# Performance work log

Measured on AMD Instinct MI355X. Metric: run time of the kernel, lower is better.

The kernel has to match this reference:

```python
import jax, jax.numpy as jnp
import numpy as np

N = 100000
E = 1600000
IN_C = 32
HID = 64
OUT_C = 32


def setup_inputs() -> dict:
    key = jax.random.key(0)
    k1, k2, k3, k4, k5, k6 = jax.random.split(key, 6)
    x = jax.random.normal(k1, (N, IN_C), dtype=jnp.float32)
    edge_index = jax.random.randint(k2, (2, E), 0, N, dtype=jnp.int64)
    # MLP params: Linear(2*in, 64) -> ReLU -> Linear(64, out)
    s1 = 1.0 / np.sqrt(2 * IN_C)
    s2 = 1.0 / np.sqrt(HID)
    W1 = jax.random.uniform(k3, (2 * IN_C, HID), jnp.float32, -s1, s1)
    b1 = jax.random.uniform(k4, (HID,), jnp.float32, -s1, s1)
    W2 = jax.random.uniform(k5, (HID, OUT_C), jnp.float32, -s2, s2)
    b2 = jax.random.uniform(k6, (OUT_C,), jnp.float32, -s2, s2)
    return {"x": x, "edge_index": edge_index, "W1": W1, "b1": b1, "W2": W2, "b2": b2}


def reference(x, edge_index, W1, b1, W2, b2):
    # PyG EdgeConv: message = nn(cat([x_i, x_j - x_i])), aggr = max over incoming edges
    src = edge_index[0]  # j (neighbor)
    dst = edge_index[1]  # i (center / target node)
    x_i = x[dst]                      # [E, C]
    x_j = x[src]                      # [E, C]
    m = jnp.concatenate([x_i, x_j - x_i], axis=-1)       # [E, 2C]
    h = jnp.maximum(m @ W1 + b1, 0.0) @ W2 + b2          # [E, OUT_C]
    out = jax.ops.segment_max(h, dst, num_segments=x.shape[0])  # [N, OUT_C]
    # nodes with no incoming edges: segment_max yields -inf; PyG fills 0
    out = jnp.where(jnp.isfinite(out), out, 0.0)
    return out
```

## Files before the change

kernel.cpp:

```cpp
#include <hip/hip_runtime.h>

typedef unsigned int u32;
typedef __attribute__((ext_vector_type(8))) _Float16 half8v;
typedef __attribute__((ext_vector_type(4))) u32 u32x4;
typedef __attribute__((ext_vector_type(4))) float f32x4;

#define NPB1 128
#define SH1  7
#define NPB2 32
#define SH2  5
#define CHP  4096

__device__ __forceinline__ u32 enc_f32(float f) {
    u32 b = __float_as_uint(f);
    return (b & 0x80000000u) ? ~b : (b | 0x80000000u);
}
__device__ __forceinline__ float dec_f32(u32 u) {
    u32 b = (u & 0x80000000u) ? (u & 0x7FFFFFFFu) : ~u;
    return __uint_as_float(b);
}
__device__ __forceinline__ u32 pk_addrelu(u32 a, u32 b) {
    u32 r;
    asm("v_pk_add_f16 %0, %1, %2\n\tv_pk_max_f16 %0, %0, 0"
        : "=v"(r) : "v"(a), "v"(b));
    return r;
}
__device__ __forceinline__ u32 pkrtz(float lo, float hi) {
    auto h = __builtin_amdgcn_cvt_pkrtz(lo, hi);
    return __builtin_bit_cast(u32, h);
}

__global__ __launch_bounds__(256) void k_pq_hist(
    const float* __restrict__ x, const float* __restrict__ W1, const float* __restrict__ b1,
    const int* __restrict__ ei,
    u32* __restrict__ Pb, u32* __restrict__ Qb, u32* __restrict__ g1,
    int N, int E, int NSB1, int npc)
{
    __shared__ u32 smem[4224];
    int tid = threadIdx.x;
    int bid = (int)blockIdx.x;

    if (bid < npc) {
        u32* cnt = smem;
        for (int s = tid; s < NSB1; s += 256) cnt[s] = 0;
        __syncthreads();
        int s0 = bid * CHP, end = min(E, s0 + CHP);
        int nq = (end - s0) >> 2;
        const int4* d4p = (const int4*)(ei + (size_t)E + s0);
        for (int qi = tid; qi < nq; qi += 256) {
            int4 d4 = d4p[qi];
            atomicAdd(&cnt[d4.x >> SH1], 1u);
            atomicAdd(&cnt[d4.y >> SH1], 1u);
            atomicAdd(&cnt[d4.z >> SH1], 1u);
            atomicAdd(&cnt[d4.w >> SH1], 1u);
        }
        __syncthreads();
        for (int s = tid; s < NSB1; s += 256) g1[(size_t)s * npc + bid] = cnt[s];
        return;
    }

    float* sWTa = (float*)smem;
    float* sWTb = (float*)smem + 2048;
    for (int idx = tid; idx < 2048; idx += 256) {
        int j = idx >> 5, k = idx & 31;
        float a = W1[k * 64 + j];
        float b = W1[(k + 32) * 64 + j];
        sWTa[j * 32 + k] = a - b;
        sWTb[j * 32 + k] = b;
    }
    __syncthreads();

    int blk = bid - npc;
    int n = blk * 256 + tid;

    u32 pw[32], qw[32];
    if (n < N) {
        float xr[32];
        const float4* x4 = reinterpret_cast<const float4*>(x + (size_t)n * 32);
#pragma unroll
        for (int q = 0; q < 8; ++q) {
            float4 v = x4[q];
            xr[4 * q] = v.x; xr[4 * q + 1] = v.y; xr[4 * q + 2] = v.z; xr[4 * q + 3] = v.w;
        }
        for (int j0 = 0; j0 < 64; j0 += 2) {
            float pv[2], qv[2];
#pragma unroll
            for (int m = 0; m < 2; ++m) {
                int j = j0 + m;
                float a = b1[j], q = 0.f;
                const f32x4* wa4 = (const f32x4*)(sWTa + j * 32);
                const f32x4* wb4 = (const f32x4*)(sWTb + j * 32);
#pragma unroll
                for (int k4 = 0; k4 < 8; ++k4) {
                    f32x4 wa = wa4[k4];
                    f32x4 wb = wb4[k4];
#pragma unroll
                    for (int e = 0; e < 4; ++e) {
                        a = fmaf(xr[4 * k4 + e], wa[e], a);
                        q = fmaf(xr[4 * k4 + e], wb[e], q);
                    }
                }
                pv[m] = a; qv[m] = q;
            }
            pw[j0 >> 1] = pkrtz(pv[0], pv[1]);
            qw[j0 >> 1] = pkrtz(qv[0], qv[1]);
        }
    }
    __syncthreads();

    u32* sP = smem;
    u32* sQ = smem + 2112;
    for (int r = 0; r < 4; ++r) {
        if ((tid >> 6) == r && n < N) {
            int row = tid & 63;
#pragma unroll
            for (int i = 0; i < 32; ++i) {
                sP[row * 33 + i] = pw[i];
                sQ[row * 33 + i] = qw[i];
            }
        }
        __syncthreads();
        int nodebase = blk * 256 + r * 64;
        size_t wbase = (size_t)nodebase * 32;
        for (int w = tid; w < 2048; w += 256) {
            int node = nodebase + (w >> 5);
            if (node < N) {
                u32 v = sP[(w >> 5) * 33 + (w & 31)];
                u32 u = sQ[(w >> 5) * 33 + (w & 31)];
                Pb[wbase + w] = v;
                Qb[wbase + w] = u;
            }
        }
        __syncthreads();
    }
}

__global__ __launch_bounds__(256) void k_scan1(const u32* __restrict__ deg, u32* __restrict__ cursor,
                                               u32* __restrict__ bsum, int M) {
    __shared__ u32 sh[256];
    int t = threadIdx.x;
    int base = blockIdx.x * 2048 + t * 8;
    u32 v[8];
    if (base + 7 < M) {
        uint4 a = *reinterpret_cast<const uint4*>(deg + base);
        uint4 b = *reinterpret_cast<const uint4*>(deg + base + 4);
        v[0] = a.x; v[1] = a.y; v[2] = a.z; v[3] = a.w;
        v[4] = b.x; v[5] = b.y; v[6] = b.z; v[7] = b.w;
    } else {
#pragma unroll
        for (int i = 0; i < 8; ++i) v[i] = (base + i < M) ? deg[base + i] : 0;
    }
    u32 s = 0;
#pragma unroll
    for (int i = 0; i < 8; ++i) s += v[i];
    sh[t] = s; __syncthreads();
    u32 acc = s;
    for (int off = 1; off < 256; off <<= 1) {
        u32 add = (t >= off) ? sh[t - off] : 0;
        __syncthreads();
        acc += add; sh[t] = acc;
        __syncthreads();
    }
    u32 run = acc - s;
#pragma unroll
    for (int i = 0; i < 8; ++i) {
        if (base + i < M) cursor[base + i] = run;
        run += v[i];
    }
    if (t == 255) bsum[blockIdx.x] = acc;
}

__global__ __launch_bounds__(256) void k_scan2(const u32* __restrict__ bsum, u32* __restrict__ bsumX, int nb) {
    __shared__ u32 sh[256];
    int t = threadIdx.x;
    u32 v = (t < nb) ? bsum[t] : 0;
    sh[t] = v; __syncthreads();
    u32 acc = v;
    for (int off = 1; off < 256; off <<= 1) {
        u32 add = (t >= off) ? sh[t - off] : 0;
        __syncthreads();
        acc += add; sh[t] = acc;
        __syncthreads();
    }
    if (t < nb) bsumX[t] = acc - v;
}

__global__ __launch_bounds__(1024) void k_sp1(const int* __restrict__ ei,
                                              const u32* __restrict__ g1cur, const u32* __restrict__ bsumX1,
                                              u32* __restrict__ sorted, int E, int NSB1, int npc) {
    __shared__ u32 sb[1024], cnt[1024];
    int tid = threadIdx.x;
    int c = (int)blockIdx.x;
    for (int s = tid; s < NSB1; s += 1024) {
        size_t idx = (size_t)s * npc + c;
        sb[s] = g1cur[idx] + bsumX1[idx >> 11];
        cnt[s] = 0;
    }
    __syncthreads();
    int s0 = c * CHP, end = min(E, s0 + CHP);
    int nq = (end - s0) >> 2;
    const int4* d4p = (const int4*)(ei + (size_t)E + s0);
    const int4* s4p = (const int4*)(ei + s0);
    for (int qi = tid; qi < nq; qi += 1024) {
        int4 d4 = d4p[qi];
        int4 s4 = s4p[qi];
        int dd[4] = {d4.x, d4.y, d4.z, d4.w};
        int ss[4] = {s4.x, s4.y, s4.z, s4.w};
#pragma unroll
        for (int u = 0; u < 4; ++u) {
            int s = dd[u] >> SH1;
            u32 r = atomicAdd(&cnt[s], 1u);
            sorted[sb[s] + r] = (u32)ss[u] | ((u32)(dd[u] & (NPB1 - 1)) << 17);
        }
    }
}

__global__ __launch_bounds__(256) void k_sp2(const u32* __restrict__ sorted,
                                             const u32* __restrict__ g1cur, const u32* __restrict__ bsumX1,
                                             u32* __restrict__ sorted2, u32* __restrict__ base32,
                                             int E, int NSB1, int npc) {
    __shared__ u32 sb[4];
    __shared__ u32 cnt[4];
    int b = (int)blockIdx.x;
    int tid = threadIdx.x;

    size_t i0 = (size_t)b * npc;
    u32 start = g1cur[i0] + bsumX1[i0 >> 11];
    u32 bend;
    if (b + 1 < NSB1) {
        size_t i1 = (size_t)(b + 1) * npc;
        bend = g1cur[i1] + bsumX1[i1 >> 11];
    } else {
        bend = (u32)E;
    }

    if (tid < 4) cnt[tid] = 0;
    __syncthreads();

    for (u32 i = start + tid; i < bend; i += 256) {
        u32 rec = sorted[i];
        atomicAdd(&cnt[(rec >> 22) & 3u], 1u);
    }
    __syncthreads();

    if (tid == 0) {
        u32 run = start;
#pragma unroll
        for (int q = 0; q < 4; ++q) {
            sb[q] = run;
            base32[b * 4 + q] = run;
            run += cnt[q];
            cnt[q] = 0;
        }
    }
    __syncthreads();

    for (u32 i0b = start; i0b < bend; i0b += 256) {
        u32 i = i0b + tid;
        bool vld = i < bend;
        u32 rec = vld ? sorted[i] : 0u;
        int q = vld ? (int)((rec >> 22) & 3u) : -1;
#pragma unroll
        for (int qq = 0; qq < 4; ++qq) {
            unsigned long long m = __ballot(q == qq);
            if (m) {
                int prefix = __popcll(m & ((1ull << (tid & 63)) - 1ull));
                u32 wb;
                if ((tid & 63) == 0) wb = atomicAdd(&cnt[qq], (u32)__popcll(m));
                wb = __shfl(wb, 0, 64);
                if (q == qq) sorted2[sb[qq] + wb + prefix] = rec & 0x3FFFFFu;
            }
        }
    }
}

__global__ __launch_bounds__(512) void k_bucket(
    const u32* __restrict__ Pb, const u32* __restrict__ Qb,
    const u32* __restrict__ sorted2, const u32* __restrict__ base32,
    const float* __restrict__ W2, const float* __restrict__ b2,
    float* __restrict__ out, int E, int N, int NSB2)
{
    __shared__ u32 agg[NPB2 * 32];
    __shared__ u32 sPb[NPB2 * 32];
    int b = (int)blockIdx.x;
    int tid = threadIdx.x;
    int nodebase = b << SH2;

    for (int i = tid; i < NPB2 * 32; i += 512) agg[i] = 0u;
    for (int i = tid; i < NPB2 * 32; i += 512) {
        int loc = i >> 5, w = i & 31;
        int node = nodebase + loc;
        u32 v = (node < N) ? Pb[(size_t)node * 32 + w] : 0u;
        sPb[loc * 32 + ((((w >> 2) ^ (loc & 7)) << 2) | (w & 3))] = v;
    }

    int lane = tid & 63;
    int wid = tid >> 6;
    int n = lane & 15;
    int kc = lane >> 4;

    half8v b00, b01, b10, b11;
#pragma unroll
    for (int j = 0; j < 8; ++j) {
        int k = kc * 8 + j;
        b00[j] = (_Float16)W2[k * 32 + n];
        b01[j] = (_Float16)W2[(k + 32) * 32 + n];
        b10[j] = (_Float16)W2[k * 32 + n + 16];
        b11[j] = (_Float16)W2[(k + 32) * 32 + n + 16];
    }

    u32 start = base32[b];
    u32 bend  = (b + 1 < NSB2) ? base32[b + 1] : (u32)E;
    int ntiles = ((int)(bend - start) + 15) >> 4;

    __syncthreads();

    int t = wid;
    u32 slotA = start + (u32)t * 16u + (u32)n;
    u32 recA = 0;
    uint4 qA0, qA1;
    if (t < ntiles) {
        u32 sl = slotA < bend ? slotA : bend - 1;
        recA = sorted2[sl];
        int src = (int)(recA & 0x1FFFFu);
        const u32* qr = Qb + (size_t)src * 32;
        qA0 = *(const uint4*)(qr + kc * 4);
        qA1 = *(const uint4*)(qr + 16 + kc * 4);
    }

    for (; t < ntiles; t += 8) {
        u32 slotB = start + (u32)(t + 8) * 16u + (u32)n;
        u32 slB = slotB < bend ? slotB : bend - 1;
        u32 recB = sorted2[slB];
        int srcB = (int)(recB & 0x1FFFFu);
        const u32* qrB = Qb + (size_t)srcB * 32;
        uint4 qB0 = *(const uint4*)(qrB + kc * 4);
        uint4 qB1 = *(const uint4*)(qrB + 16 + kc * 4);

        bool valid = slotA < bend;
        int locA = (int)(recA >> 17);
        int local = valid ? locA : -1;

        const u32* pr = sPb + locA * 32;
        uint4 pA0 = *(const uint4*)(pr + ((kc ^ (locA & 7)) << 2));
        uint4 pA1 = *(const uint4*)(pr + (((4 + kc) ^ (locA & 7)) << 2));

        u32x4 aw0, aw1;
        aw0[0] = pk_addrelu(pA0.x, qA0.x);
        aw0[1] = pk_addrelu(pA0.y, qA0.y);
        aw0[2] = pk_addrelu(pA0.z, qA0.z);
        aw0[3] = pk_addrelu(pA0.w, qA0.w);
        aw1[0] = pk_addrelu(pA1.x, qA1.x);
        aw1[1] = pk_addrelu(pA1.y, qA1.y);
        aw1[2] = pk_addrelu(pA1.z, qA1.z);
        aw1[3] = pk_addrelu(pA1.w, qA1.w);
        half8v a0 = __builtin_bit_cast(half8v, aw0);
        half8v a1 = __builtin_bit_cast(half8v, aw1);

        f32x4 d0 = {0.f, 0.f, 0.f, 0.f};
        f32x4 d1 = {0.f, 0.f, 0.f, 0.f};
        d0 = __builtin_amdgcn_mfma_f32_16x16x32_f16(a0, b00, d0, 0, 0, 0);
        d0 = __builtin_amdgcn_mfma_f32_16x16x32_f16(a1, b01, d0, 0, 0, 0);
        d1 = __builtin_amdgcn_mfma_f32_16x16x32_f16(a0, b10, d1, 0, 0, 0);
        d1 = __builtin_amdgcn_mfma_f32_16x16x32_f16(a1, b11, d1, 0, 0, 0);

#pragma unroll
        for (int i = 0; i < 4; ++i) {
            int r = kc * 4 + i;
            int lr = __shfl(local, r, 64);
            if (lr >= 0) {
                int sw = (lr & 1) << 4;
                atomicMax(&agg[(lr << 5) + (n ^ sw)], enc_f32(d0[i]));
                atomicMax(&agg[(lr << 5) + ((n + 16) ^ sw)], enc_f32(d1[i]));
            }
        }

        slotA = slotB; recA = recB;
        qA0 = qB0; qA1 = qB1;
    }

    __syncthreads();
    for (int i = tid; i < NPB2 * 32; i += 512) {
        int local = i >> 5, c = i & 31;
        int node = nodebase + local;
        if (node < N) {
            u32 u = agg[(local << 5) + (c ^ ((local & 1) << 4))];
            out[(size_t)node * 32 + c] = u ? (dec_f32(u) + b2[c]) : 0.f;
        }
    }
}

__global__ __launch_bounds__(256) void fb_edge(const float* __restrict__ x, const int* __restrict__ ei,
                                               const float* __restrict__ W1, const float* __restrict__ b1,
                                               const float* __restrict__ W2, const float* __restrict__ b2,
                                               u32* __restrict__ out, int E) {
    int e = blockIdx.x * 256 + threadIdx.x;
    if (e >= E) return;
    int src = ei[e], dst = ei[E + e];
    float m[64];
    const float4* xi4 = reinterpret_cast<const float4*>(x + (size_t)dst * 32);
    const float4* xj4 = reinterpret_cast<const float4*>(x + (size_t)src * 32);
#pragma unroll
    for (int q = 0; q < 8; ++q) {
        float4 a = xi4[q], b = xj4[q];
        m[q * 4] = a.x; m[q * 4 + 1] = a.y; m[q * 4 + 2] = a.z; m[q * 4 + 3] = a.w;
        m[32 + q * 4] = b.x - a.x; m[32 + q * 4 + 1] = b.y - a.y;
        m[32 + q * 4 + 2] = b.z - a.z; m[32 + q * 4 + 3] = b.w - a.w;
    }
    float acc[32];
#pragma unroll
    for (int c = 0; c < 32; ++c) acc[c] = b2[c];
    for (int j = 0; j < 64; ++j) {
        float h = b1[j];
#pragma unroll
        for (int k = 0; k < 64; ++k) h = fmaf(m[k], W1[k * 64 + j], h);
        h = fmaxf(h, 0.0f);
#pragma unroll
        for (int c = 0; c < 32; ++c) acc[c] = fmaf(h, W2[j * 32 + c], acc[c]);
    }
    u32* o = out + (size_t)dst * 32;
#pragma unroll
    for (int c = 0; c < 32; ++c) atomicMax(o + c, enc_f32(acc[c]));
}
__global__ __launch_bounds__(256) void fb_decode(u32* __restrict__ buf, int n) {
    int i = blockIdx.x * 256 + threadIdx.x;
    if (i >= n) return;
    u32 u = buf[i];
    reinterpret_cast<float*>(buf)[i] = u ? dec_f32(u) : 0.f;
}

extern "C" void kernel_launch(void* const* d_in, const int* in_sizes, int n_in,
                              void* d_out, int out_size, void* d_ws, size_t ws_size,
                              hipStream_t stream) {
    const float* x  = (const float*)d_in[0];
    const int*   ei = (const int*)d_in[1];
    const float* W1 = (const float*)d_in[2];
    const float* b1 = (const float*)d_in[3];
    const float* W2 = (const float*)d_in[4];
    const float* b2 = (const float*)d_in[5];

    int N = in_sizes[0] / 32;
    int E = in_sizes[1] / 2;
    int NSB1 = (N + NPB1 - 1) >> SH1;
    int NSB2 = NSB1 * 4;
    int npc = (E + CHP - 1) / CHP;
    int M1  = NSB1 * npc;
    int nb1 = (M1 + 2047) / 2048;

    char* ws = (char*)d_ws;
    size_t off = 0;
    auto alloc = [&](size_t bytes) { char* p = ws + off; off += (bytes + 255) & ~(size_t)255; return p; };
    u32*   Pb      = (u32*)alloc((size_t)N * 32 * 4);
    u32*   Qb      = (u32*)alloc((size_t)N * 32 * 4);
    u32*   g1      = (u32*)alloc((size_t)M1 * 4);
    u32*   g1cur   = (u32*)alloc((size_t)M1 * 4);
    u32*   bsum1   = (u32*)alloc(256 * 4);
    u32*   bsumX1  = (u32*)alloc(256 * 4);
    u32*   base32  = (u32*)alloc((size_t)(NSB2 + 1) * 4);
    u32*   sorted  = (u32*)alloc((size_t)E * 4);
    u32*   sorted2 = (u32*)alloc((size_t)E * 4);
    bool fits = (off <= ws_size) && (NSB1 <= 1024) &&
                (N < (1 << 17)) && ((E & 3) == 0) && (nb1 <= 256);

    if (!fits) {
        hipMemsetAsync(d_out, 0, (size_t)out_size * 4, stream);
        int be = (E + 255) / 256;
        fb_edge<<<be, 256, 0, stream>>>(x, ei, W1, b1, W2, b2, (u32*)d_out, E);
        fb_decode<<<(out_size + 255) / 256, 256, 0, stream>>>((u32*)d_out, out_size);
        return;
    }

    int pq_blocks = (N + 255) / 256;
    k_pq_hist<<<npc + pq_blocks, 256, 0, stream>>>(x, W1, b1, ei, Pb, Qb, g1, N, E, NSB1, npc);

    k_scan1<<<nb1, 256, 0, stream>>>(g1, g1cur, bsum1, M1);
    k_scan2<<<1, 256, 0, stream>>>(bsum1, bsumX1, nb1);

    k_sp1<<<npc, 1024, 0, stream>>>(ei, g1cur, bsumX1, sorted, E, NSB1, npc);

    k_sp2<<<NSB1, 256, 0, stream>>>(sorted, g1cur, bsumX1, sorted2, base32, E, NSB1, npc);

    k_bucket<<<NSB2, 512, 0, stream>>>(Pb, Qb, sorted2, base32, W2, b2,
                                       (float*)d_out, E, N, NSB2);
}
```

Baseline: 110.5 us.

## Replace two-pass bucket sort with single-pass 32-node bucketing

The destination bucketing now sorts edges straight into 32-node buckets in one scatter pass, removing the secondary k_sp2 refinement kernel and its extra sorted2 buffer. The histogram grows from about 782 to about 3125 buckets, so the count matrix and scan are four times larger. k_scan2 gains a loop to handle more than 256 partial sums. This saves one read and one write over the edge list plus a launch, at the cost of more LDS atomics spread over more counters, a larger g1 transpose and scan, and a bigger per-block shared array in k_sp1 that may lower occupancy.

Result: slower. 120.1 us (+8.7%).

```diff
diff --git a/kernel.cpp b/kernel.cpp
--- a/kernel.cpp
+++ b/kernel.cpp
@@ -5,11 +5,9 @@
 typedef __attribute__((ext_vector_type(4))) u32 u32x4;
 typedef __attribute__((ext_vector_type(4))) float f32x4;
 
-#define NPB1 128
-#define SH1  7
-#define NPB2 32
-#define SH2  5
-#define CHP  4096
+#define NPB 32
+#define SH  5
+#define CHP 4096
 
 __device__ __forceinline__ u32 enc_f32(float f) {
     u32 b = __float_as_uint(f);
@@ -34,7 +32,7 @@
     const float* __restrict__ x, const float* __restrict__ W1, const float* __restrict__ b1,
     const int* __restrict__ ei,
     u32* __restrict__ Pb, u32* __restrict__ Qb, u32* __restrict__ g1,
-    int N, int E, int NSB1, int npc)
+    int N, int E, int NSB, int npc)
 {
     __shared__ u32 smem[4224];
     int tid = threadIdx.x;
@@ -42,20 +40,20 @@
 
     if (bid < npc) {
         u32* cnt = smem;
-        for (int s = tid; s < NSB1; s += 256) cnt[s] = 0;
+        for (int s = tid; s < NSB; s += 256) cnt[s] = 0;
         __syncthreads();
         int s0 = bid * CHP, end = min(E, s0 + CHP);
         int nq = (end - s0) >> 2;
         const int4* d4p = (const int4*)(ei + (size_t)E + s0);
         for (int qi = tid; qi < nq; qi += 256) {
             int4 d4 = d4p[qi];
-            atomicAdd(&cnt[d4.x >> SH1], 1u);
-            atomicAdd(&cnt[d4.y >> SH1], 1u);
-            atomicAdd(&cnt[d4.z >> SH1], 1u);
-            atomicAdd(&cnt[d4.w >> SH1], 1u);
-        }
-        __syncthreads();
-        for (int s = tid; s < NSB1; s += 256) g1[(size_t)s * npc + bid] = cnt[s];
+            atomicAdd(&cnt[d4.x >> SH], 1u);
+            atomicAdd(&cnt[d4.y >> SH], 1u);
+            atomicAdd(&cnt[d4.z >> SH], 1u);
+            atomicAdd(&cnt[d4.w >> SH], 1u);
+        }
+        __syncthreads();
+        for (int s = tid; s < NSB; s += 256) g1[(size_t)s * npc + bid] = cnt[s];
         return;
     }
 
@@ -172,26 +170,35 @@
 
 __global__ __launch_bounds__(256) void k_scan2(const u32* __restrict__ bsum, u32* __restrict__ bsumX, int nb) {
     __shared__ u32 sh[256];
+    __shared__ u32 carry;
     int t = threadIdx.x;
-    u32 v = (t < nb) ? bsum[t] : 0;
-    sh[t] = v; __syncthreads();
-    u32 acc = v;
-    for (int off = 1; off < 256; off <<= 1) {
-        u32 add = (t >= off) ? sh[t - off] : 0;
-        __syncthreads();
-        acc += add; sh[t] = acc;
-        __syncthreads();
-    }
-    if (t < nb) bsumX[t] = acc - v;
+    if (t == 0) carry = 0;
+    __syncthreads();
+    for (int r0 = 0; r0 < nb; r0 += 256) {
+        int i = r0 + t;
+        u32 v = (i < nb) ? bsum[i] : 0;
+        sh[t] = v; __syncthreads();
+        u32 acc = v;
+        for (int off = 1; off < 256; off <<= 1) {
+            u32 add = (t >= off) ? sh[t - off] : 0;
+            __syncthreads();
+            acc += add; sh[t] = acc;
+            __syncthreads();
+        }
+        if (i < nb) bsumX[i] = carry + acc - v;
+        __syncthreads();
+        if (t == 255) carry += acc;
+        __syncthreads();
+    }
 }
 
 __global__ __launch_bounds__(1024) void k_sp1(const int* __restrict__ ei,
                                               const u32* __restrict__ g1cur, const u32* __restrict__ bsumX1,
-                                              u32* __restrict__ sorted, int E, int NSB1, int npc) {
-    __shared__ u32 sb[1024], cnt[1024];
+                                              u32* __restrict__ sorted, int E, int NSB, int npc) {
+    __shared__ u32 sb[3328], cnt[3328];
     int tid = threadIdx.x;
     int c = (int)blockIdx.x;
-    for (int s = tid; s < NSB1; s += 1024) {
+    for (int s = tid; s < NSB; s += 1024) {
         size_t idx = (size_t)s * npc + c;
         sb[s] = g1cur[idx] + bsumX1[idx >> 11];
         cnt[s] = 0;
@@ -208,86 +215,27 @@
         int ss[4] = {s4.x, s4.y, s4.z, s4.w};
 #pragma unroll
         for (int u = 0; u < 4; ++u) {
-            int s = dd[u] >> SH1;
+            int s = dd[u] >> SH;
             u32 r = atomicAdd(&cnt[s], 1u);
-            sorted[sb[s] + r] = (u32)ss[u] | ((u32)(dd[u] & (NPB1 - 1)) << 17);
-        }
-    }
-}
-
-__global__ __launch_bounds__(256) void k_sp2(const u32* __restrict__ sorted,
-                                             const u32* __restrict__ g1cur, const u32* __restrict__ bsumX1,
-                                             u32* __restrict__ sorted2, u32* __restrict__ base32,
-                                             int E, int NSB1, int npc) {
-    __shared__ u32 sb[4];
-    __shared__ u32 cnt[4];
+            sorted[sb[s] + r] = (u32)ss[u] | ((u32)(dd[u] & (NPB - 1)) << 17);
+        }
+    }
+}
+
+__global__ __launch_bounds__(512) void k_bucket(
+    const u32* __restrict__ Pb, const u32* __restrict__ Qb,
+    const u32* __restrict__ sorted, const u32* __restrict__ g1cur, const u32* __restrict__ bsumX1,
+    const float* __restrict__ W2, const float* __restrict__ b2,
+    float* __restrict__ out, int E, int N, int NSB, int npc)
+{
+    __shared__ u32 agg[NPB * 32];
+    __shared__ u32 sPb[NPB * 32];
     int b = (int)blockIdx.x;
     int tid = threadIdx.x;
-
-    size_t i0 = (size_t)b * npc;
-    u32 start = g1cur[i0] + bsumX1[i0 >> 11];
-    u32 bend;
-    if (b + 1 < NSB1) {
-        size_t i1 = (size_t)(b + 1) * npc;
-        bend = g1cur[i1] + bsumX1[i1 >> 11];
-    } else {
-        bend = (u32)E;
-    }
-
-    if (tid < 4) cnt[tid] = 0;
-    __syncthreads();
-
-    for (u32 i = start + tid; i < bend; i += 256) {
-        u32 rec = sorted[i];
-        atomicAdd(&cnt[(rec >> 22) & 3u], 1u);
-    }
-    __syncthreads();
-
-    if (tid == 0) {
-        u32 run = start;
-#pragma unroll
-        for (int q = 0; q < 4; ++q) {
-            sb[q] = run;
-            base32[b * 4 + q] = run;
-            run += cnt[q];
-            cnt[q] = 0;
-        }
-    }
-    __syncthreads();
-
-    for (u32 i0b = start; i0b < bend; i0b += 256) {
-        u32 i = i0b + tid;
-        bool vld = i < bend;
-        u32 rec = vld ? sorted[i] : 0u;
-        int q = vld ? (int)((rec >> 22) & 3u) : -1;
-#pragma unroll
-        for (int qq = 0; qq < 4; ++qq) {
-            unsigned long long m = __ballot(q == qq);
-            if (m) {
-                int prefix = __popcll(m & ((1ull << (tid & 63)) - 1ull));
-                u32 wb;
-                if ((tid & 63) == 0) wb = atomicAdd(&cnt[qq], (u32)__popcll(m));
-                wb = __shfl(wb, 0, 64);
-                if (q == qq) sorted2[sb[qq] + wb + prefix] = rec & 0x3FFFFFu;
-            }
-        }
-    }
-}
-
-__global__ __launch_bounds__(512) void k_bucket(
-    const u32* __restrict__ Pb, const u32* __restrict__ Qb,
-    const u32* __restrict__ sorted2, const u32* __restrict__ base32,
-    const float* __restrict__ W2, const float* __restrict__ b2,
-    float* __restrict__ out, int E, int N, int NSB2)
-{
-    __shared__ u32 agg[NPB2 * 32];
-    __shared__ u32 sPb[NPB2 * 32];
-    int b = (int)blockIdx.x;
-    int tid = threadIdx.x;
-    int nodebase = b << SH2;
-
-    for (int i = tid; i < NPB2 * 32; i += 512) agg[i] = 0u;
-    for (int i = tid; i < NPB2 * 32; i += 512) {
+    int nodebase = b << SH;
+
+    for (int i = tid; i < NPB * 32; i += 512) agg[i] = 0u;
+    for (int i = tid; i < NPB * 32; i += 512) {
         int loc = i >> 5, w = i & 31;
         int node = nodebase + loc;
         u32 v = (node < N) ? Pb[(size_t)node * 32 + w] : 0u;
@@ -309,8 +257,15 @@
         b11[j] = (_Float16)W2[(k + 32) * 32 + n + 16];
     }
 
-    u32 start = base32[b];
-    u32 bend  = (b + 1 < NSB2) ? base32[b + 1] : (u32)E;
+    size_t i0 = (size_t)b * npc;
+    u32 start = g1cur[i0] + bsumX1[i0 >> 11];
+    u32 bend;
+    if (b + 1 < NSB) {
+        size_t i1 = (size_t)(b + 1) * npc;
+        bend = g1cur[i1] + bsumX1[i1 >> 11];
+    } else {
+        bend = (u32)E;
+    }
     int ntiles = ((int)(bend - start) + 15) >> 4;
 
     __syncthreads();
@@ -321,7 +276,7 @@
     uint4 qA0, qA1;
     if (t < ntiles) {
         u32 sl = slotA < bend ? slotA : bend - 1;
-        recA = sorted2[sl];
+        recA = sorted[sl];
         int src = (int)(recA & 0x1FFFFu);
         const u32* qr = Qb + (size_t)src * 32;
         qA0 = *(const uint4*)(qr + kc * 4);
@@ -331,7 +286,7 @@
     for (; t < ntiles; t += 8) {
         u32 slotB = start + (u32)(t + 8) * 16u + (u32)n;
         u32 slB = slotB < bend ? slotB : bend - 1;
-        u32 recB = sorted2[slB];
+        u32 recB = sorted[slB];
         int srcB = (int)(recB & 0x1FFFFu);
         const u32* qrB = Qb + (size_t)srcB * 32;
         uint4 qB0 = *(const uint4*)(qrB + kc * 4);
@@ -380,7 +335,7 @@
     }
 
     __syncthreads();
-    for (int i = tid; i < NPB2 * 32; i += 512) {
+    for (int i = tid; i < NPB * 32; i += 512) {
         int local = i >> 5, c = i & 31;
         int node = nodebase + local;
         if (node < N) {
@@ -441,10 +396,9 @@
 
     int N = in_sizes[0] / 32;
     int E = in_sizes[1] / 2;
-    int NSB1 = (N + NPB1 - 1) >> SH1;
-    int NSB2 = NSB1 * 4;
+    int NSB = (N + NPB - 1) >> SH;
     int npc = (E + CHP - 1) / CHP;
-    int M1  = NSB1 * npc;
+    int M1  = (int)((size_t)NSB * npc);
     int nb1 = (M1 + 2047) / 2048;
 
     char* ws = (char*)d_ws;
@@ -454,13 +408,11 @@
     u32*   Qb      = (u32*)alloc((size_t)N * 32 * 4);
     u32*   g1      = (u32*)alloc((size_t)M1 * 4);
     u32*   g1cur   = (u32*)alloc((size_t)M1 * 4);
-    u32*   bsum1   = (u32*)alloc(256 * 4);
-    u32*   bsumX1  = (u32*)alloc(256 * 4);
-    u32*   base32  = (u32*)alloc((size_t)(NSB2 + 1) * 4);
+    u32*   bsum1   = (u32*)alloc(1024 * 4);
+    u32*   bsumX1  = (u32*)alloc(1024 * 4);
     u32*   sorted  = (u32*)alloc((size_t)E * 4);
-    u32*   sorted2 = (u32*)alloc((size_t)E * 4);
-    bool fits = (off <= ws_size) && (NSB1 <= 1024) &&
-                (N < (1 << 17)) && ((E & 3) == 0) && (nb1 <= 256);
+    bool fits = (off <= ws_size) && (NSB <= 3328) &&
+                (N < (1 << 17)) && ((E & 3) == 0) && (nb1 <= 1024);
 
     if (!fits) {
         hipMemsetAsync(d_out, 0, (size_t)out_size * 4, stream);
@@ -471,15 +423,13 @@
     }
 
     int pq_blocks = (N + 255) / 256;
-    k_pq_hist<<<npc + pq_blocks, 256, 0, stream>>>(x, W1, b1, ei, Pb, Qb, g1, N, E, NSB1, npc);
+    k_pq_hist<<<npc + pq_blocks, 256, 0, stream>>>(x, W1, b1, ei, Pb, Qb, g1, N, E, NSB, npc);
 
     k_scan1<<<nb1, 256, 0, stream>>>(g1, g1cur, bsum1, M1);
     k_scan2<<<1, 256, 0, stream>>>(bsum1, bsumX1, nb1);
 
-    k_sp1<<<npc, 1024, 0, stream>>>(ei, g1cur, bsumX1, sorted, E, NSB1, npc);
-
-    k_sp2<<<NSB1, 256, 0, stream>>>(sorted, g1cur, bsumX1, sorted2, base32, E, NSB1, npc);
-
-    k_bucket<<<NSB2, 512, 0, stream>>>(Pb, Qb, sorted2, base32, W2, b2,
-                                       (float*)d_out, E, N, NSB2);
-}
+    k_sp1<<<npc, 1024, 0, stream>>>(ei, g1cur, bsumX1, sorted, E, NSB, npc);
+
+    k_bucket<<<NSB, 512, 0, stream>>>(Pb, Qb, sorted, g1cur, bsumX1, W2, b2,
+                                      (float*)d_out, E, N, NSB, npc);
+}
```
